# Optimization experiments

Measured on AMD Instinct MI355X. Metric: run time of the kernel, lower is better.

Reference implementation:

```python
import jax, jax.numpy as jnp
import numpy as np


def setup_inputs() -> dict:
    key = jax.random.key(0)
    N, C, H, W, D = 4, 128, 48, 48, 48
    x = jax.random.normal(key, (N, C, H, W, D), dtype=jnp.float32)
    return {"x": x}


def reference(x) -> jnp.ndarray:
    # Channel self-attention over flattened spatial dims.
    N, C, H, W, D = x.shape
    q = x.reshape(N, C, -1)                      # [N, C, S]
    # energy[n, i, j] = <channel i, channel j>
    energy = jnp.einsum('ncs,nms->ncm', q, q)    # [N, C, C]
    # max-subtract trick (note: softmax of (max - energy), NOT energy - max)
    energy_new = jnp.max(energy, axis=-1, keepdims=True) - energy
    attention = jax.nn.softmax(energy_new, axis=-1)  # [N, C, C]
    out = jnp.einsum('ncm,nms->ncs', attention, q)   # [N, C, S]
    return out.reshape(N, C, H, W, D)
```

## Files before the change

kernel.cpp:

```cpp
#include <hip/hip_runtime.h>
#include <math.h>


static constexpr int CN = 128;
static constexpr int SN = 110592;
static constexpr int NB = 4;

static constexpr int GB = 64;
static constexpr int GSL = SN / GB;
static constexpr int GCH = GSL / 64;

static constexpr int PB = 432;
static constexpr int PCH = 4;

typedef float  f32x4  __attribute__((ext_vector_type(4)));
typedef short  bf16x8 __attribute__((ext_vector_type(8)));
typedef unsigned short u16x4 __attribute__((ext_vector_type(4)));

__device__ __forceinline__ unsigned int cvtpk(float a, float b) {
    unsigned int r;
    asm("v_cvt_pk_bf16_f32 %0, %1, %2" : "=v"(r) : "v"(a), "v"(b));
    return r;
}
__device__ __forceinline__ unsigned short f2bh(float v) {
    unsigned int u = __float_as_uint(v);
    return (unsigned short)((u + 0x7fffu + ((u >> 16) & 1u)) >> 16);
}

__device__ __forceinline__ bf16x8 ldsfrag(const unsigned short* base, int row, int kbyte, int pitchB) {
    const char* p = reinterpret_cast<const char*>(base) + row * pitchB + (kbyte ^ ((row & 7) << 4));
    return *reinterpret_cast<const bf16x8*>(p);
}
__device__ __forceinline__ f32x4 mm(bf16x8 a, bf16x8 b, f32x4 c) {
    return __builtin_amdgcn_mfma_f32_16x16x32_bf16(a, b, c, 0, 0, 0);
}

template <bool ATOMIC>
__global__ __launch_bounds__(512, 1) void gram_mfma(const float* __restrict__ x,
                                                    float* __restrict__ dst) {
    __shared__ __align__(16) unsigned short lh[2][CN * 64];
    __shared__ __align__(16) unsigned short ll[2][CN * 64];
    const int bx = blockIdx.x, n = blockIdx.y;
    const int tid = threadIdx.x;
    const int lane = tid & 63;
    const int w = tid >> 6;
    const int wr = (w >> 1) & 1, wc = w & 1;
    const int kh = w >> 2;
    const int ra = lane & 15, kg = lane >> 4;

    const int c  = tid >> 2;
    const int ks = (tid & 3) << 4;
    const float* gq = x + (size_t)n * CN * SN + (size_t)c * SN + bx * GSL;

    f32x4 acc[4][4];
#pragma unroll
    for (int a = 0; a < 4; ++a)
#pragma unroll
        for (int b = 0; b < 4; ++b) acc[a][b] = (f32x4){0.f, 0.f, 0.f, 0.f};

    float4 st[4];
    auto load_chunk = [&](int t) {
        const float4* p = reinterpret_cast<const float4*>(gq + t * 64 + ks);
        st[0] = p[0]; st[1] = p[1]; st[2] = p[2]; st[3] = p[3];
    };

    auto stage = [&](int buf) {
        unsigned int hw[8], lw[8];
#pragma unroll
        for (int r = 0; r < 4; ++r) {
            const unsigned int hp0 = cvtpk(st[r].x, st[r].y);
            const unsigned int hp1 = cvtpk(st[r].z, st[r].w);
            const unsigned int lp0 = cvtpk(st[r].x - __uint_as_float(hp0 << 16),
                                           st[r].y - __uint_as_float(hp0 & 0xffff0000u));
            const unsigned int lp1 = cvtpk(st[r].z - __uint_as_float(hp1 << 16),
                                           st[r].w - __uint_as_float(hp1 & 0xffff0000u));
            hw[r * 2] = hp0; hw[r * 2 + 1] = hp1;
            lw[r * 2] = lp0; lw[r * 2 + 1] = lp1;
        }
        char* ph = reinterpret_cast<char*>(lh[buf]) + c * 128;
        char* pl = reinterpret_cast<char*>(ll[buf]) + c * 128;
        const int sw = (c & 7) << 4;
        const int k2 = ks * 2;
        *reinterpret_cast<uint4*>(ph + (k2 ^ sw))        = make_uint4(hw[0], hw[1], hw[2], hw[3]);
        *reinterpret_cast<uint4*>(ph + ((k2 + 16) ^ sw)) = make_uint4(hw[4], hw[5], hw[6], hw[7]);
        *reinterpret_cast<uint4*>(pl + (k2 ^ sw))        = make_uint4(lw[0], lw[1], lw[2], lw[3]);
        *reinterpret_cast<uint4*>(pl + ((k2 + 16) ^ sw)) = make_uint4(lw[4], lw[5], lw[6], lw[7]);
    };

    auto compute = [&](int buf) {
        const unsigned short* LH = lh[buf];
        const unsigned short* LL = ll[buf];
        const int kb = (kh << 6) + (kg << 4);
        bf16x8 ah[4], al[4], bh[4], bl[4];
#pragma unroll
        for (int it = 0; it < 4; ++it) {
            const int row = wr * 64 + it * 16 + ra;
            ah[it] = ldsfrag(LH, row, kb, 128);
            al[it] = ldsfrag(LL, row, kb, 128);
        }
#pragma unroll
        for (int jt = 0; jt < 4; ++jt) {
            const int row = wc * 64 + jt * 16 + ra;
            bh[jt] = ldsfrag(LH, row, kb, 128);
            bl[jt] = ldsfrag(LL, row, kb, 128);
        }
#pragma unroll
        for (int it = 0; it < 4; ++it)
#pragma unroll
            for (int jt = 0; jt < 4; ++jt) {
                acc[it][jt] = mm(ah[it], bh[jt], acc[it][jt]);
                acc[it][jt] = mm(ah[it], bl[jt], acc[it][jt]);
                acc[it][jt] = mm(al[it], bh[jt], acc[it][jt]);
            }
    };

    load_chunk(0);
    for (int t = 0; t < GCH; ++t) {
        stage(t & 1);
        if (t < GCH - 1) load_chunk(t + 1);
        __syncthreads();
        compute(t & 1);
    }

    __syncthreads();
    float* ex = (w & 2) ? reinterpret_cast<float*>(ll[w & 1])
                        : reinterpret_cast<float*>(lh[w & 1]);
    if (w >= 4) {
#pragma unroll
        for (int it = 0; it < 4; ++it)
#pragma unroll
            for (int jt = 0; jt < 4; ++jt)
                *reinterpret_cast<f32x4*>(ex + (it * 4 + jt) * 256 + lane * 4) = acc[it][jt];
    }
    __syncthreads();
    if (w < 4) {
#pragma unroll
        for (int it = 0; it < 4; ++it)
#pragma unroll
            for (int jt = 0; jt < 4; ++jt)
                acc[it][jt] += *reinterpret_cast<const f32x4*>(ex + (it * 4 + jt) * 256 + lane * 4);

        const int q4 = kg << 2;
        if (!ATOMIC) {
            float* P = dst + (size_t)(n * GB + bx) * (CN * CN);
#pragma unroll
            for (int it = 0; it < 4; ++it)
#pragma unroll
                for (int jt = 0; jt < 4; ++jt)
#pragma unroll
                    for (int q = 0; q < 4; ++q)
                        __builtin_nontemporal_store(acc[it][jt][q],
                            &P[(wr * 64 + it * 16 + q4 + q) * CN + wc * 64 + jt * 16 + ra]);
        } else {
            float* E = dst + (size_t)n * CN * CN;
#pragma unroll
            for (int it = 0; it < 4; ++it)
#pragma unroll
                for (int jt = 0; jt < 4; ++jt)
#pragma unroll
                    for (int q = 0; q < 4; ++q)
                        atomicAdd(&E[(wr * 64 + it * 16 + q4 + q) * CN + wc * 64 + jt * 16 + ra], acc[it][jt][q]);
        }
    }
}

template <bool REDUCE>
__global__ __launch_bounds__(256) void finish_kernel(const float* __restrict__ src,
                                                     unsigned short* __restrict__ att_h) {
    __shared__ float red[8][64];
    const int i = blockIdx.x, n = blockIdx.y;
    const int tid = threadIdx.x;
    const int lane = tid & 63, w = tid >> 6;
    float e0 = 0.f, e1 = 0.f;
    if (REDUCE) {
        const float* p = src + (size_t)n * GB * (CN * CN) + i * CN;
#pragma unroll
        for (int k = 0; k < GB / 4; ++k) {
            const size_t o = (size_t)(w * (GB / 4) + k) * (CN * CN);
            e0 += __builtin_nontemporal_load(&p[o + lane]);
            e1 += __builtin_nontemporal_load(&p[o + lane + 64]);
        }
        red[w * 2][lane]     = e0;
        red[w * 2 + 1][lane] = e1;
        __syncthreads();
        if (w != 0) return;
        e0 = ((red[0][lane] + red[2][lane]) + (red[4][lane] + red[6][lane]));
        e1 = ((red[1][lane] + red[3][lane]) + (red[5][lane] + red[7][lane]));
    } else {
        if (w != 0) return;
        const float* E = src + ((size_t)n * CN + i) * CN;
        e0 = E[lane]; e1 = E[lane + 64];
    }
    float m = fminf(e0, e1);
#pragma unroll
    for (int off = 32; off > 0; off >>= 1) m = fminf(m, __shfl_xor(m, off));
    const float p0 = expf(m - e0);
    const float p1 = expf(m - e1);
    float s = p0 + p1;
#pragma unroll
    for (int off = 32; off > 0; off >>= 1) s += __shfl_xor(s, off);
    const float inv = 1.f / s;
    const size_t o = ((size_t)n * CN + i) * CN;
    att_h[o + lane]      = f2bh(p0 * inv);
    att_h[o + lane + 64] = f2bh(p1 * inv);
}

__global__ __launch_bounds__(512, 4) void pv_mfma(const float* __restrict__ x,
                                                  const unsigned short* __restrict__ att_h,
                                                  float* __restrict__ out) {
    __shared__ __align__(16) unsigned short qh[2][64 * CN];
    const int bx = blockIdx.x, n = blockIdx.y;
    const int tid = threadIdx.x;
    const int lane = tid & 63;
    const int w = tid >> 6;
    const int ra = lane & 15, kg = lane >> 4;

    bf16x8 a_h[4];
    {
        const size_t rowoff = ((size_t)n * CN + w * 16 + ra) * CN + kg * 8;
        const unsigned short* Ah = att_h + rowoff;
#pragma unroll
        for (int kk = 0; kk < 4; ++kk)
            a_h[kk] = *reinterpret_cast<const bf16x8*>(Ah + kk * 32);
    }

    const int j0 = (tid >> 4) * 4;
    const int s0 = (tid & 15) * 4;
    const float* gx = x + (size_t)n * CN * SN;
    const int sbase = bx * (PCH * 64);

    f32x4 st[4];
    auto load_chunk = [&](int sb) {
#pragma unroll
        for (int r = 0; r < 4; ++r)
            st[r] = *reinterpret_cast<const f32x4*>(gx + (size_t)(j0 + r) * SN + sb + s0);
    };

    auto stage = [&](int buf) {
        char* base = reinterpret_cast<char*>(qh[buf]);
#pragma unroll
        for (int r = 0; r < 4; ++r) {
            uint2 hv;
            hv.x = cvtpk(st[0][r], st[1][r]);
            hv.y = cvtpk(st[2][r], st[3][r]);
            const int s = s0 + r;
            const int off = s * 256 + ((j0 * 2) ^ ((s & 7) << 4));
            *reinterpret_cast<uint2*>(base + off) = hv;
        }
    };

    auto compute = [&](int buf, int sb) {
        const unsigned short* Q = qh[buf];
#pragma unroll
        for (int stile = 0; stile < 4; ++stile) {
            f32x4 acc = (f32x4){0.f, 0.f, 0.f, 0.f};
            const int srow = stile * 16 + ra;
#pragma unroll
            for (int kk = 0; kk < 4; ++kk) {
                const int kb = kk * 64 + (kg << 4);
                bf16x8 bh = ldsfrag(Q, srow, kb, 256);
                acc = mm(a_h[kk], bh, acc);
            }
            float* o = out + ((size_t)n * CN + w * 16 + (kg << 2)) * SN + sb + stile * 16 + ra;
#pragma unroll
            for (int q = 0; q < 4; ++q)
                __builtin_nontemporal_store(acc[q], o + (size_t)q * SN);
        }
    };

    load_chunk(sbase);
    for (int t = 0; t < PCH; ++t) {
        stage(t & 1);
        if (t < PCH - 1) load_chunk(sbase + (t + 1) * 64);
        __syncthreads();
        compute(t & 1, sbase + t * 64);
    }
}

extern "C" void kernel_launch(void* const* d_in, const int* in_sizes, int n_in,
                              void* d_out, int out_size, void* d_ws, size_t ws_size,
                              hipStream_t stream) {
    (void)in_sizes; (void)n_in; (void)out_size;
    const float* x = (const float*)d_in[0];
    float* out = (float*)d_out;

    float* energy = (float*)d_ws;
    unsigned short* att_h = (unsigned short*)(energy + (size_t)NB * CN * CN);
    float* part = (float*)(att_h + (size_t)NB * CN * CN);
    const size_t need =
        (size_t)NB * CN * CN * sizeof(float) +
        (size_t)NB * CN * CN * sizeof(unsigned short) +
        (size_t)NB * GB * CN * CN * sizeof(float);

    if (ws_size >= need) {
        gram_mfma<false><<<dim3(GB, NB), 512, 0, stream>>>(x, part);
        finish_kernel<true><<<dim3(CN, NB), 256, 0, stream>>>(part, att_h);
    } else {
        hipMemsetAsync(energy, 0, (size_t)NB * CN * CN * sizeof(float), stream);
        gram_mfma<true><<<dim3(GB, NB), 512, 0, stream>>>(x, energy);
        finish_kernel<false><<<dim3(CN, NB), 256, 0, stream>>>(energy, att_h);
    }
    pv_mfma<<<dim3(PB, NB), 512, 0, stream>>>(x, att_h, out);
}
```

Baseline: 134.1 us.

## Retile Gram kernel: 2x4 warp grid, single LDS buffer, two blocks per CU

```diff
diff --git a/kernel.cpp b/kernel.cpp
--- a/kernel.cpp
+++ b/kernel.cpp
@@ -15,7 +15,6 @@
 
 typedef float  f32x4  __attribute__((ext_vector_type(4)));
 typedef short  bf16x8 __attribute__((ext_vector_type(8)));
-typedef unsigned short u16x4 __attribute__((ext_vector_type(4)));
 
 __device__ __forceinline__ unsigned int cvtpk(float a, float b) {
     unsigned int r;
@@ -36,27 +35,26 @@
 }
 
 template <bool ATOMIC>
-__global__ __launch_bounds__(512, 1) void gram_mfma(const float* __restrict__ x,
+__global__ __launch_bounds__(512, 2) void gram_mfma(const float* __restrict__ x,
                                                     float* __restrict__ dst) {
-    __shared__ __align__(16) unsigned short lh[2][CN * 64];
-    __shared__ __align__(16) unsigned short ll[2][CN * 64];
+    __shared__ __align__(16) unsigned short lh[CN * 64];
+    __shared__ __align__(16) unsigned short ll[CN * 64];
     const int bx = blockIdx.x, n = blockIdx.y;
     const int tid = threadIdx.x;
     const int lane = tid & 63;
     const int w = tid >> 6;
-    const int wr = (w >> 1) & 1, wc = w & 1;
-    const int kh = w >> 2;
+    const int wr = w >> 2, wc = w & 3;
     const int ra = lane & 15, kg = lane >> 4;
 
     const int c  = tid >> 2;
     const int ks = (tid & 3) << 4;
     const float* gq = x + (size_t)n * CN * SN + (size_t)c * SN + bx * GSL;
 
-    f32x4 acc[4][4];
+    f32x4 acc[4][2];
 #pragma unroll
     for (int a = 0; a < 4; ++a)
 #pragma unroll
-        for (int b = 0; b < 4; ++b) acc[a][b] = (f32x4){0.f, 0.f, 0.f, 0.f};
+        for (int b = 0; b < 2; ++b) acc[a][b] = (f32x4){0.f, 0.f, 0.f, 0.f};
 
     float4 st[4];
     auto load_chunk = [&](int t) {
@@ -64,7 +62,7 @@
         st[0] = p[0]; st[1] = p[1]; st[2] = p[2]; st[3] = p[3];
     };
 
-    auto stage = [&](int buf) {
+    auto stage = [&]() {
         unsigned int hw[8], lw[8];
 #pragma unroll
         for (int r = 0; r < 4; ++r) {
@@ -77,8 +75,8 @@
             hw[r * 2] = hp0; hw[r * 2 + 1] = hp1;
             lw[r * 2] = lp0; lw[r * 2 + 1] = lp1;
         }
-        char* ph = reinterpret_cast<char*>(lh[buf]) + c * 128;
-        char* pl = reinterpret_cast<char*>(ll[buf]) + c * 128;
+        char* ph = reinterpret_cast<char*>(lh) + c * 128;
+        char* pl = reinterpret_cast<char*>(ll) + c * 128;
         const int sw = (c & 7) << 4;
         const int k2 = ks * 2;
         *reinterpret_cast<uint4*>(ph + (k2 ^ sw))        = make_uint4(hw[0], hw[1], hw[2], hw[3]);
@@ -87,80 +85,63 @@
         *reinterpret_cast<uint4*>(pl + ((k2 + 16) ^ sw)) = make_uint4(lw[4], lw[5], lw[6], lw[7]);
     };
 
-    auto compute = [&](int buf) {
-        const unsigned short* LH = lh[buf];
-        const unsigned short* LL = ll[buf];
-        const int kb = (kh << 6) + (kg << 4);
-        bf16x8 ah[4], al[4], bh[4], bl[4];
-#pragma unroll
-        for (int it = 0; it < 4; ++it) {
-            const int row = wr * 64 + it * 16 + ra;
-            ah[it] = ldsfrag(LH, row, kb, 128);
-            al[it] = ldsfrag(LL, row, kb, 128);
-        }
-#pragma unroll
-        for (int jt = 0; jt < 4; ++jt) {
-            const int row = wc * 64 + jt * 16 + ra;
-            bh[jt] = ldsfrag(LH, row, kb, 128);
-            bl[jt] = ldsfrag(LL, row, kb, 128);
-        }
-#pragma unroll
-        for (int it = 0; it < 4; ++it)
-#pragma unroll
-            for (int jt = 0; jt < 4; ++jt) {
-                acc[it][jt] = mm(ah[it], bh[jt], acc[it][jt]);
-                acc[it][jt] = mm(ah[it], bl[jt], acc[it][jt]);
-                acc[it][jt] = mm(al[it], bh[jt], acc[it][jt]);
+    auto compute = [&]() {
+#pragma unroll
+        for (int kk = 0; kk < 2; ++kk) {
+            const int kb = kk * 64 + (kg << 4);
+            bf16x8 ah[4], al[4], bh[2], bl[2];
+#pragma unroll
+            for (int it = 0; it < 4; ++it) {
+                const int row = wr * 64 + it * 16 + ra;
+                ah[it] = ldsfrag(lh, row, kb, 128);
+                al[it] = ldsfrag(ll, row, kb, 128);
             }
+#pragma unroll
+            for (int jt = 0; jt < 2; ++jt) {
+                const int row = wc * 32 + jt * 16 + ra;
+                bh[jt] = ldsfrag(lh, row, kb, 128);
+                bl[jt] = ldsfrag(ll, row, kb, 128);
+            }
+#pragma unroll
+            for (int it = 0; it < 4; ++it)
+#pragma unroll
+                for (int jt = 0; jt < 2; ++jt) {
+                    acc[it][jt] = mm(ah[it], bh[jt], acc[it][jt]);
+                    acc[it][jt] = mm(ah[it], bl[jt], acc[it][jt]);
+                    acc[it][jt] = mm(al[it], bh[jt], acc[it][jt]);
+                }
+        }
     };
 
     load_chunk(0);
     for (int t = 0; t < GCH; ++t) {
-        stage(t & 1);
+        __syncthreads();
+        stage();
         if (t < GCH - 1) load_chunk(t + 1);
         __syncthreads();
-        compute(t & 1);
-    }
-
-    __syncthreads();
-    float* ex = (w & 2) ? reinterpret_cast<float*>(ll[w & 1])
-                        : reinterpret_cast<float*>(lh[w & 1]);
-    if (w >= 4) {
+        compute();
+    }
+
+    const int q4 = kg << 2;
+    if (!ATOMIC) {
+        float* P = dst + (size_t)(n * GB + bx) * (CN * CN);
 #pragma unroll
         for (int it = 0; it < 4; ++it)
 #pragma unroll
-            for (int jt = 0; jt < 4; ++jt)
-                *reinterpret_cast<f32x4*>(ex + (it * 4 + jt) * 256 + lane * 4) = acc[it][jt];
-    }
-    __syncthreads();
-    if (w < 4) {
+            for (int jt = 0; jt < 2; ++jt)
+#pragma unroll
+                for (int q = 0; q < 4; ++q)
+                    __builtin_nontemporal_store(acc[it][jt][q],
+                        &P[(wr * 64 + it * 16 + q4 + q) * CN + wc * 32 + jt * 16 + ra]);
+    } else {
+        float* E = dst + (size_t)n * CN * CN;
 #pragma unroll
         for (int it = 0; it < 4; ++it)
 #pragma unroll
-            for (int jt = 0; jt < 4; ++jt)
-                acc[it][jt] += *reinterpret_cast<const f32x4*>(ex + (it * 4 + jt) * 256 + lane * 4);
-
-        const int q4 = kg << 2;
-        if (!ATOMIC) {
-            float* P = dst + (size_t)(n * GB + bx) * (CN * CN);
-#pragma unroll
-            for (int it = 0; it < 4; ++it)
-#pragma unroll
-                for (int jt = 0; jt < 4; ++jt)
-#pragma unroll
-                    for (int q = 0; q < 4; ++q)
-                        __builtin_nontemporal_store(acc[it][jt][q],
-                            &P[(wr * 64 + it * 16 + q4 + q) * CN + wc * 64 + jt * 16 + ra]);
-        } else {
-            float* E = dst + (size_t)n * CN * CN;
-#pragma unroll
-            for (int it = 0; it < 4; ++it)
-#pragma unroll
-                for (int jt = 0; jt < 4; ++jt)
-#pragma unroll
-                    for (int q = 0; q < 4; ++q)
-                        atomicAdd(&E[(wr * 64 + it * 16 + q4 + q) * CN + wc * 64 + jt * 16 + ra], acc[it][jt][q]);
-        }
+            for (int jt = 0; jt < 2; ++jt)
+#pragma unroll
+                for (int q = 0; q < 4; ++q)
+                    atomicAdd(&E[(wr * 64 + it * 16 + q4 + q) * CN + wc * 32 + jt * 16 + ra], acc[it][jt][q]);
     }
 }
 
```

New measurement: 134.9 us. No clear change (+0.5%).
